# Kernel optimization log

Hardware: AMD Instinct MI355X
Metric: run time of the kernel (lower is better)

## Reference

```python
import jax, jax.numpy as jnp
import numpy as np

B, S, C_IN = 32, 4096, 21
D_MODEL = 512
M, TAU = 7, 1
K = M + 1                 # kernel_size = 8
NUM_KERNELS = 74          # 73 depthwise kernels + 1 'final' kernel
PAD = M * TAU             # left zero-pad = 7 -> num_windows == S
PROJ_IN = 73 * C_IN + 1   # 1534


def setup_inputs() -> dict:
    key = jax.random.key(0)
    k_x, k_k, k_w, k_b = jax.random.split(key, 4)
    x = jax.random.normal(k_x, (B, S, C_IN), dtype=jnp.float32)
    kernels = jax.random.normal(k_k, (NUM_KERNELS, K), dtype=jnp.float32)
    # nn.Conv1d(PROJ_IN, D_MODEL, 1): weight [D_MODEL, PROJ_IN, 1] -> squeeze kernel dim
    fan_in = PROJ_IN
    bound = 1.0 / np.sqrt(fan_in)
    proj_w = jax.random.uniform(k_w, (D_MODEL, PROJ_IN), dtype=jnp.float32, minval=-bound, maxval=bound)
    proj_b = jax.random.uniform(k_b, (D_MODEL,), dtype=jnp.float32, minval=-bound, maxval=bound)
    return {"x": x, "kernels": kernels, "proj_w": proj_w, "proj_b": proj_b}


def reference(x, kernels, proj_w, proj_b):
    # x: [B, S, C]. Left-pad the time axis with zeros (ConstantPad1d((PAD, 0), 0)).
    xp = jnp.pad(x, ((0, 0), (PAD, 0), (0, 0)))  # [B, S+PAD, C]
    num_windows = x.shape[1]  # (S+PAD) - K + 1 == S when tau == 1
    # Gather sliding windows: [B, W, K, C]
    idx = jnp.arange(num_windows)[:, None] * TAU + jnp.arange(K)[None, :]
    windows = xp[:, idx, :]
    # 73 depthwise kernels, each applied to every channel. Torch concat order is
    # per-kernel blocks of c_in channels: [k0 c0..cC, k1 c0..cC, ...].
    main = jnp.einsum('bwkc,nk->bwnc', windows, kernels[: NUM_KERNELS - 1])
    main = main.reshape(x.shape[0], num_windows, (NUM_KERNELS - 1) * x.shape[2])
    # Final feature: last kernel applied to one channel (torch uses a random
    # channel; fixed to channel 0 here for determinism).
    final = jnp.einsum('bwk,k->bw', windows[:, :, :, 0], kernels[NUM_KERNELS - 1])[..., None]
    combined = jnp.concatenate([main, final], axis=2)  # [B, W, 73*C+1]
    # 1x1 Conv1d projection over channels -> [B, D_MODEL, W]
    out = jnp.einsum('bwc,dc->bdw', combined, proj_w) + proj_b[None, :, None]
    return out
```

## Files before the change

kernel.cpp:

```cpp
#include <hip/hip_runtime.h>

#define B_    32
#define S_    4096
#define CIN   21
#define DM    512
#define KW    8
#define NK    74
#define PROJIN 1534

#define CP    24
#define KSEG  192
#define WSTR  200
#define DT    128
#define WT    128
#define SROWS 136

typedef __attribute__((ext_vector_type(8))) short bf16x8;
typedef __attribute__((ext_vector_type(4))) float f32x4;

__device__ __forceinline__ unsigned short f2bf_rne(float x) {
  unsigned u = __float_as_uint(x);
  unsigned r = (u + 0x7FFFu + ((u >> 16) & 1u)) >> 16;
  return (unsigned short)r;
}
__device__ __forceinline__ float bf2f(unsigned short b) {
  return __uint_as_float(((unsigned)b) << 16);
}

__global__ __launch_bounds__(256) void build_weff(
    const float* __restrict__ kernels, const float* __restrict__ proj_w,
    unsigned short* __restrict__ wh, unsigned short* __restrict__ wl) {
  __shared__ float pw[PROJIN];
  __shared__ float kk[NK * KW];
  const int d = blockIdx.x, tid = threadIdx.x;
  for (int i = tid; i < PROJIN; i += 256) pw[i] = proj_w[d * PROJIN + i];
  for (int i = tid; i < NK * KW; i += 256) kk[i] = kernels[i];
  __syncthreads();
  if (tid < KSEG) {
    const int k = tid / CP, c = tid % CP;
    float acc = 0.f;
    if (c < CIN) {
      #pragma unroll 1
      for (int n = 0; n < 73; ++n)
        acc = fmaf(pw[n * CIN + c], kk[n * KW + k], acc);
      if (c == 0) acc = fmaf(pw[PROJIN - 1], kk[73 * KW + k], acc);
    }
    const unsigned short h = f2bf_rne(acc);
    wh[d * KSEG + tid] = h;
    wl[d * KSEG + tid] = f2bf_rne(acc - bf2f(h));
  }
}

__global__ __launch_bounds__(256, 2) void conv_mfma(
    const float* __restrict__ x, const unsigned short* __restrict__ wh,
    const unsigned short* __restrict__ wl, const float* __restrict__ proj_b,
    float* __restrict__ out) {
  __shared__ __align__(16) unsigned short Wt[DT * WSTR];
  __shared__ __align__(16) unsigned short Xh[SROWS * CP];
  __shared__ __align__(16) unsigned short Xl[SROWS * CP];
  __shared__ float bl[DT];

  const int tid = threadIdx.x;
  const int blk = blockIdx.x;
  const int dt = blk & 3;
  const int wt = (blk >> 2) & 31;
  const int b  = blk >> 7;
  const int d0 = dt * DT;
  const int w0 = wt * WT;

  const float* xb = x + (size_t)b * (S_ * CIN);
  for (int i = tid; i < SROWS * CP; i += 256) {
    const int s = i / CP, cc = i - s * CP;
    const int wg = w0 - 7 + s;
    float v = 0.f;
    if (cc < CIN && wg >= 0 && wg < S_) v = xb[wg * CIN + cc];
    const unsigned short h = f2bf_rne(v);
    Xh[i] = h;
    Xl[i] = f2bf_rne(v - bf2f(h));
  }
  for (int i = tid; i < DT * (KSEG / 8); i += 256) {
    const int r = i / (KSEG / 8), j = i - r * (KSEG / 8);
    *(bf16x8*)&Wt[r * WSTR + j * 8] =
        *(const bf16x8*)&wh[(size_t)(d0 + r) * KSEG + j * 8];
  }
  if (tid < DT) bl[tid] = proj_b[d0 + tid];
  __syncthreads();

  const int l     = tid & 63;
  const int wave  = tid >> 6;
  const int l15   = l & 15;
  const int q     = l >> 4;
  const int q8    = q * 8;
  const int wavew = (wave & 1) * 64;
  const int waved = (wave >> 1) * 64;

  int koffS[6];
  #pragma unroll
  for (int s = 0; s < 6; ++s) {
    const int k0 = 32 * s + q8;
    const int k = k0 / CP, c0 = k0 - k * CP;
    koffS[s] = k * CP + c0;
  }
  int xbaseS[4], wbaseS[4];
  #pragma unroll
  for (int m = 0; m < 4; ++m) xbaseS[m] = (wavew + m * 16 + l15) * CP;
  #pragma unroll
  for (int n = 0; n < 4; ++n) wbaseS[n] = (waved + n * 16 + l15) * WSTR + q8;

  f32x4 acc[4][4] = {};

  #pragma unroll
  for (int s = 0; s < 6; ++s) {
    bf16x8 fw[4], fh[4], fl[4];
    #pragma unroll
    for (int n = 0; n < 4; ++n)
      fw[n] = *(const bf16x8*)&Wt[wbaseS[n] + s * 32];
    #pragma unroll
    for (int m = 0; m < 4; ++m) {
      fh[m] = *(const bf16x8*)&Xh[xbaseS[m] + koffS[s]];
      fl[m] = *(const bf16x8*)&Xl[xbaseS[m] + koffS[s]];
    }
    #pragma unroll
    for (int m = 0; m < 4; ++m)
      #pragma unroll
      for (int n = 0; n < 4; ++n) {
        acc[m][n] = __builtin_amdgcn_mfma_f32_16x16x32_bf16(
            fh[m], fw[n], acc[m][n], 0, 0, 0);
        acc[m][n] = __builtin_amdgcn_mfma_f32_16x16x32_bf16(
            fl[m], fw[n], acc[m][n], 0, 0, 0);
      }
  }
  __syncthreads();
  for (int i = tid; i < DT * (KSEG / 8); i += 256) {
    const int r = i / (KSEG / 8), j = i - r * (KSEG / 8);
    *(bf16x8*)&Wt[r * WSTR + j * 8] =
        *(const bf16x8*)&wl[(size_t)(d0 + r) * KSEG + j * 8];
  }
  __syncthreads();
  #pragma unroll
  for (int s = 0; s < 6; ++s) {
    bf16x8 fw[4], fh[4];
    #pragma unroll
    for (int n = 0; n < 4; ++n)
      fw[n] = *(const bf16x8*)&Wt[wbaseS[n] + s * 32];
    #pragma unroll
    for (int m = 0; m < 4; ++m)
      fh[m] = *(const bf16x8*)&Xh[xbaseS[m] + koffS[s]];
    #pragma unroll
    for (int m = 0; m < 4; ++m)
      #pragma unroll
      for (int n = 0; n < 4; ++n)
        acc[m][n] = __builtin_amdgcn_mfma_f32_16x16x32_bf16(
            fh[m], fw[n], acc[m][n], 0, 0, 0);
  }

  const size_t ob = (size_t)b * DM * S_;
  #pragma unroll
  for (int n = 0; n < 4; ++n) {
    const int d = d0 + waved + n * 16 + l15;
    const float bias = bl[waved + n * 16 + l15];
    #pragma unroll
    for (int m = 0; m < 4; ++m) {
      const int w = w0 + wavew + m * 16 + q * 4;
      f32x4 v = acc[m][n];
      v = v + bias;
      *(f32x4*)&out[ob + (size_t)d * S_ + w] = v;
    }
  }
}

extern "C" void kernel_launch(void* const* d_in, const int* in_sizes, int n_in,
                              void* d_out, int out_size, void* d_ws, size_t ws_size,
                              hipStream_t stream) {
  const float* x       = (const float*)d_in[0];
  const float* kernels = (const float*)d_in[1];
  const float* proj_w  = (const float*)d_in[2];
  const float* proj_b  = (const float*)d_in[3];
  float* out = (float*)d_out;

  unsigned short* weff_hi = (unsigned short*)d_ws;
  unsigned short* weff_lo = weff_hi + (size_t)DM * KSEG;

  build_weff<<<DM, 256, 0, stream>>>(kernels, proj_w, weff_hi, weff_lo);
  conv_mfma<<<B_ * 32 * 4, 256, 0, stream>>>(x, weff_hi, weff_lo, proj_b, out);
}
```

Measured before the change: 399.6 us.

## Stream weight fragments from global memory and enlarge the time tile with an interleaved X layout

The convolution kernel now covers 256 time steps per block instead of 128, and each wave handles all 128 output channels instead of 64. Weight hi/lo fragments are loaded straight from global memory (L2-cached) into registers, so the shared-memory weight staging and the two mid-kernel barriers are gone. The X tile is stored in a channel-group-major layout that puts hi and lo together. All three bf16 split products now run in a single loop. Each thread holds twice as many accumulators, which raises register pressure and may limit occupancy, and every wave refetches weights from global memory.

```diff
diff --git a/kernel.cpp b/kernel.cpp
--- a/kernel.cpp
+++ b/kernel.cpp
@@ -7,13 +7,13 @@
 #define KW    8
 #define NK    74
 #define PROJIN 1534
-
 #define CP    24
 #define KSEG  192
-#define WSTR  200
-#define DT    128
-#define WT    128
-#define SROWS 136
+
+#define WT    256
+#define DTB   128
+#define SROWS 263
+#define R_    265
 
 typedef __attribute__((ext_vector_type(8))) short bf16x8;
 typedef __attribute__((ext_vector_type(4))) float f32x4;
@@ -51,117 +51,94 @@
   }
 }
 
-__global__ __launch_bounds__(256, 2) void conv_mfma(
+__global__ __launch_bounds__(256, 2) void conv_mfma2(
     const float* __restrict__ x, const unsigned short* __restrict__ wh,
     const unsigned short* __restrict__ wl, const float* __restrict__ proj_b,
     float* __restrict__ out) {
-  __shared__ __align__(16) unsigned short Wt[DT * WSTR];
-  __shared__ __align__(16) unsigned short Xh[SROWS * CP];
-  __shared__ __align__(16) unsigned short Xl[SROWS * CP];
-  __shared__ float bl[DT];
+  __shared__ __align__(16) unsigned short Xt[2 * 3 * R_ * 8];
 
   const int tid = threadIdx.x;
   const int blk = blockIdx.x;
   const int dt = blk & 3;
-  const int wt = (blk >> 2) & 31;
-  const int b  = blk >> 7;
-  const int d0 = dt * DT;
+  const int wt = (blk >> 2) & 15;
+  const int b  = blk >> 6;
+  const int d0 = dt * DTB;
   const int w0 = wt * WT;
 
   const float* xb = x + (size_t)b * (S_ * CIN);
   for (int i = tid; i < SROWS * CP; i += 256) {
-    const int s = i / CP, cc = i - s * CP;
+    const int s = i / CP, c = i - s * CP;
     const int wg = w0 - 7 + s;
     float v = 0.f;
-    if (cc < CIN && wg >= 0 && wg < S_) v = xb[wg * CIN + cc];
+    if (c < CIN && wg >= 0) v = xb[wg * CIN + c];
     const unsigned short h = f2bf_rne(v);
-    Xh[i] = h;
-    Xl[i] = f2bf_rne(v - bf2f(h));
+    const unsigned short lo = f2bf_rne(v - bf2f(h));
+    const int g = c >> 3, e = c & 7;
+    Xt[(g * R_ + s) * 8 + e] = h;
+    Xt[((3 + g) * R_ + s) * 8 + e] = lo;
   }
-  for (int i = tid; i < DT * (KSEG / 8); i += 256) {
-    const int r = i / (KSEG / 8), j = i - r * (KSEG / 8);
-    *(bf16x8*)&Wt[r * WSTR + j * 8] =
-        *(const bf16x8*)&wh[(size_t)(d0 + r) * KSEG + j * 8];
-  }
-  if (tid < DT) bl[tid] = proj_b[d0 + tid];
   __syncthreads();
 
-  const int l     = tid & 63;
-  const int wave  = tid >> 6;
-  const int l15   = l & 15;
-  const int q     = l >> 4;
-  const int q8    = q * 8;
-  const int wavew = (wave & 1) * 64;
-  const int waved = (wave >> 1) * 64;
+  const int l    = tid & 63;
+  const int wave = tid >> 6;
+  const int l15  = l & 15;
+  const int q    = l >> 4;
+  const int q8   = q * 8;
 
-  int koffS[6];
+  int koff[6];
   #pragma unroll
   for (int s = 0; s < 6; ++s) {
     const int k0 = 32 * s + q8;
     const int k = k0 / CP, c0 = k0 - k * CP;
-    koffS[s] = k * CP + c0;
+    koff[s] = (c0 >> 3) * R_ + k;
   }
-  int xbaseS[4], wbaseS[4];
-  #pragma unroll
-  for (int m = 0; m < 4; ++m) xbaseS[m] = (wavew + m * 16 + l15) * CP;
-  #pragma unroll
-  for (int n = 0; n < 4; ++n) wbaseS[n] = (waved + n * 16 + l15) * WSTR + q8;
+  const int rowb = wave * 64 + l15;
+  const int wrow = (d0 + l15) * KSEG + q8;
 
-  f32x4 acc[4][4] = {};
+  f32x4 acc[4][8] = {};
 
   #pragma unroll
   for (int s = 0; s < 6; ++s) {
-    bf16x8 fw[4], fh[4], fl[4];
-    #pragma unroll
-    for (int n = 0; n < 4; ++n)
-      fw[n] = *(const bf16x8*)&Wt[wbaseS[n] + s * 32];
+    bf16x8 fh[4], fl[4];
     #pragma unroll
     for (int m = 0; m < 4; ++m) {
-      fh[m] = *(const bf16x8*)&Xh[xbaseS[m] + koffS[s]];
-      fl[m] = *(const bf16x8*)&Xl[xbaseS[m] + koffS[s]];
+      const int gi = koff[s] + rowb + m * 16;
+      fh[m] = *(const bf16x8*)&Xt[gi * 8];
+      fl[m] = *(const bf16x8*)&Xt[(gi + 3 * R_) * 8];
     }
     #pragma unroll
-    for (int m = 0; m < 4; ++m)
+    for (int half = 0; half < 2; ++half) {
+      bf16x8 fwh[4], fwl[4];
       #pragma unroll
-      for (int n = 0; n < 4; ++n) {
-        acc[m][n] = __builtin_amdgcn_mfma_f32_16x16x32_bf16(
-            fh[m], fw[n], acc[m][n], 0, 0, 0);
-        acc[m][n] = __builtin_amdgcn_mfma_f32_16x16x32_bf16(
-            fl[m], fw[n], acc[m][n], 0, 0, 0);
+      for (int j = 0; j < 4; ++j) {
+        const int n = half * 4 + j;
+        const int off = wrow + n * (16 * KSEG) + s * 32;
+        fwh[j] = *(const bf16x8*)&wh[off];
+        fwl[j] = *(const bf16x8*)&wl[off];
       }
-  }
-  __syncthreads();
-  for (int i = tid; i < DT * (KSEG / 8); i += 256) {
-    const int r = i / (KSEG / 8), j = i - r * (KSEG / 8);
-    *(bf16x8*)&Wt[r * WSTR + j * 8] =
-        *(const bf16x8*)&wl[(size_t)(d0 + r) * KSEG + j * 8];
-  }
-  __syncthreads();
-  #pragma unroll
-  for (int s = 0; s < 6; ++s) {
-    bf16x8 fw[4], fh[4];
-    #pragma unroll
-    for (int n = 0; n < 4; ++n)
-      fw[n] = *(const bf16x8*)&Wt[wbaseS[n] + s * 32];
-    #pragma unroll
-    for (int m = 0; m < 4; ++m)
-      fh[m] = *(const bf16x8*)&Xh[xbaseS[m] + koffS[s]];
-    #pragma unroll
-    for (int m = 0; m < 4; ++m)
       #pragma unroll
-      for (int n = 0; n < 4; ++n)
-        acc[m][n] = __builtin_amdgcn_mfma_f32_16x16x32_bf16(
-            fh[m], fw[n], acc[m][n], 0, 0, 0);
+      for (int m = 0; m < 4; ++m)
+        #pragma unroll
+        for (int j = 0; j < 4; ++j) {
+          const int n = half * 4 + j;
+          acc[m][n] = __builtin_amdgcn_mfma_f32_16x16x32_bf16(
+              fh[m], fwh[j], acc[m][n], 0, 0, 0);
+          acc[m][n] = __builtin_amdgcn_mfma_f32_16x16x32_bf16(
+              fl[m], fwh[j], acc[m][n], 0, 0, 0);
+          acc[m][n] = __builtin_amdgcn_mfma_f32_16x16x32_bf16(
+              fh[m], fwl[j], acc[m][n], 0, 0, 0);
+        }
+    }
   }
 
   const size_t ob = (size_t)b * DM * S_;
   #pragma unroll
-  for (int n = 0; n < 4; ++n) {
-    const int d = d0 + waved + n * 16 + l15;
-    const float bias = bl[waved + n * 16 + l15];
+  for (int n = 0; n < 8; ++n) {
+    const int d = d0 + n * 16 + l15;
+    const float bias = proj_b[d];
     #pragma unroll
     for (int m = 0; m < 4; ++m) {
-      const int w = w0 + wavew + m * 16 + q * 4;
+      const int w = w0 + wave * 64 + m * 16 + q * 4;
       f32x4 v = acc[m][n];
       v = v + bias;
       *(f32x4*)&out[ob + (size_t)d * S_ + w] = v;
@@ -182,5 +159,5 @@
   unsigned short* weff_lo = weff_hi + (size_t)DM * KSEG;
 
   build_weff<<<DM, 256, 0, stream>>>(kernels, proj_w, weff_hi, weff_lo);
-  conv_mfma<<<B_ * 32 * 4, 256, 0, stream>>>(x, weff_hi, weff_lo, proj_b, out);
+  conv_mfma2<<<B_ * 16 * 4, 256, 0, stream>>>(x, weff_hi, weff_lo, proj_b, out);
 }
```

Measured after the change: 418.0 us. +4.6%, slower.
